# Optimization experiments

Hardware: AMD Instinct MI355X
Metric: run time of the kernel (lower is better)

## Reference

```python
import math
import jax, jax.numpy as jnp
import numpy as np


def get_slopes(n):
    def pow2(n):
        start = 2.0 ** (-(2.0 ** (-(math.log2(n) - 3))))
        return [start * (start ** i) for i in range(n)]
    if math.log2(n).is_integer():
        return pow2(n)
    c = 2 ** math.floor(math.log2(n))
    return pow2(c) + get_slopes(2 * c)[0::2][: n - c]


def setup_inputs() -> dict:
    key = jax.random.key(0)
    B, T, C = 2, 2048, 1024
    ks = jax.random.split(key, 9)
    std = 0.02
    n_layers = 12
    inp = {
        "x": jax.random.normal(ks[0], (B, T, C), dtype=jnp.float32),
        # weights stored as [in, out] (transpose of torch Linear.weight)
        "Wq": std * jax.random.normal(ks[1], (C, C), dtype=jnp.float32),
        "bq": jnp.zeros((C,), dtype=jnp.float32),
        "Wk": std * jax.random.normal(ks[2], (C, C), dtype=jnp.float32),
        "bk": jnp.zeros((C,), dtype=jnp.float32),
        "Wv": std * jax.random.normal(ks[3], (C, C), dtype=jnp.float32),
        "bv": jnp.zeros((C,), dtype=jnp.float32),
        # fc_resid gets std 0.02/sqrt(2*num_layers)
        "Wo": (std / math.sqrt(2 * n_layers)) * jax.random.normal(ks[4], (C, C), dtype=jnp.float32),
        "bo": jnp.zeros((C,), dtype=jnp.float32),
        "n_head": 16,
    }
    return inp


def reference(x, Wq, bq, Wk, bk, Wv, bv, Wo, bo, n_head):
    B, T, C = x.shape
    hd = C // n_head
    # QKV projections, split heads: [B, nh, T, hd]
    def proj(W, b):
        return (x @ W + b).reshape(B, T, n_head, hd).transpose(0, 2, 1, 3)
    q, k, v = proj(Wq, bq), proj(Wk, bk), proj(Wv, bv)

    # ALiBi bias: bias[h, i, j] = -slope_h * (i - j) for j <= i, -inf above diag
    slopes = jnp.asarray(get_slopes(n_head), dtype=x.dtype)  # [nh]
    idx = jnp.arange(T)
    dist = (idx[:, None] - idx[None, :]).astype(x.dtype)  # [T, T], i - j
    bias = -slopes[:, None, None] * dist  # [nh, T, T]
    causal = idx[:, None] >= idx[None, :]
    bias = jnp.where(causal[None], bias, jnp.asarray(-jnp.inf, dtype=x.dtype))

    scale = 1.0 / math.sqrt(hd)
    scores = jnp.einsum("bnqh,bnkh->bnqk", q, k) * scale + bias[None]
    att = jax.nn.softmax(scores, axis=-1)
    y = jnp.einsum("bnqk,bnkh->bnqh", att, v)  # [B, nh, T, hd]
    y = y.transpose(0, 2, 1, 3).reshape(B, T, C)
    return y @ Wo + bo
```

## Files before the change

kernel.cpp:

```cpp
#include <hip/hip_runtime.h>


typedef unsigned short u16;
typedef unsigned int u32;
typedef __attribute__((ext_vector_type(8))) short bf16x8;
typedef __attribute__((ext_vector_type(4))) float f32x4;
typedef __attribute__((ext_vector_type(4))) unsigned short u16x4;

#define MFMA16x16(A, B, C_) __builtin_amdgcn_mfma_f32_16x16x32_bf16((A), (B), (C_), 0, 0, 0)

__device__ __forceinline__ u16 f2bf(float f) {
  u32 x = __builtin_bit_cast(u32, f);
  x += 0x7fff + ((x >> 16) & 1);
  return (u16)(x >> 16);
}

__device__ __forceinline__ void gload_lds16(const u16* g, u16* l) {
  __builtin_amdgcn_global_load_lds(
      (const __attribute__((address_space(1))) void*)g,
      (__attribute__((address_space(3))) void*)l, 16, 0, 0);
}

constexpr int T = 2048, C = 1024, HD = 64;
constexpr int BT = 2 * T;

__device__ __forceinline__ bf16x8 ldsfrag(const u16* lds, int row, int kchunk) {
  return *(const bf16x8*)(lds + row * 64 + (((kchunk) ^ (row & 7)) << 3));
}

__global__ __launch_bounds__(256) void convert_x_kernel(
    const float* __restrict__ xin, u16* __restrict__ xc) {
  int i = (blockIdx.x * 256 + threadIdx.x) * 8;
  const float4 a = *(const float4*)(xin + i);
  const float4 b = *(const float4*)(xin + i + 4);
  uint4 o;
  o.x = (u32)f2bf(a.x) | ((u32)f2bf(a.y) << 16);
  o.y = (u32)f2bf(a.z) | ((u32)f2bf(a.w) << 16);
  o.z = (u32)f2bf(b.x) | ((u32)f2bf(b.y) << 16);
  o.w = (u32)f2bf(b.z) | ((u32)f2bf(b.w) << 16);
  *(uint4*)(xc + i) = o;
}

__global__ __launch_bounds__(256) void transpose4_kernel(
    const float* __restrict__ w0, const float* __restrict__ w1,
    const float* __restrict__ w2, const float* __restrict__ w3,
    u16* __restrict__ wqkvT, u16* __restrict__ woT) {
  __shared__ u16 tile[32][33];
  const int z = blockIdx.z;
  const float* in = (z == 0) ? w0 : (z == 1) ? w1 : (z == 2) ? w2 : w3;
  u16* out = (z < 3) ? (wqkvT + (size_t)z * (1u << 20)) : woT;
  int tx = threadIdx.x, ty = threadIdx.y;
  int x = blockIdx.x * 32 + tx;
#pragma unroll
  for (int i = 0; i < 4; i++) {
    int y = blockIdx.y * 32 + ty + i * 8;
    tile[ty + i * 8][tx] = f2bf(in[y * 1024 + x]);
  }
  __syncthreads();
  int xo = blockIdx.y * 32 + tx;
#pragma unroll
  for (int i = 0; i < 4; i++) {
    int yo = blockIdx.x * 32 + ty + i * 8;
    out[yo * 1024 + xo] = tile[tx][ty + i * 8];
  }
}

__global__ __launch_bounds__(256) void gemm_qkv_kernel(
    const u16* __restrict__ A, const u16* __restrict__ Bt,
    const float* __restrict__ b0, const float* __restrict__ b1,
    const float* __restrict__ b2,
    u16* __restrict__ qout, u16* __restrict__ kout, u16* __restrict__ vtout) {
  constexpr int K = 1024;
  __shared__ __align__(16) u16 As[128 * 64];
  __shared__ __align__(16) u16 Bs[128 * 64];

  const int tid = threadIdx.x;
  const int w = tid >> 6, lane = tid & 63;
  const int l15 = lane & 15, quad = lane >> 4;
  const int m0 = blockIdx.y * 128, n0 = blockIdx.x * 128;
  const int wm = (w >> 1) * 64, wn = (w & 1) * 64;
  const int gsub = (lane & 7) ^ ((lane >> 3) & 7);
  const int rsub = lane >> 3;

  f32x4 acc[4][4] = {};
  const u16* Ag = A + (size_t)m0 * K;
  const u16* Bg = Bt + (size_t)n0 * K;

  for (int k0 = 0; k0 < K; k0 += 64) {
    __syncthreads();
#pragma unroll
    for (int t = 0; t < 4; t++) {
      int rbase = w * 32 + t * 8;
      gload_lds16(Ag + (size_t)(rbase + rsub) * K + k0 + gsub * 8, As + rbase * 64);
      gload_lds16(Bg + (size_t)(rbase + rsub) * K + k0 + gsub * 8, Bs + rbase * 64);
    }
    __syncthreads();
#pragma unroll
    for (int ks = 0; ks < 2; ks++) {
      bf16x8 af[4], bf[4];
#pragma unroll
      for (int mi = 0; mi < 4; mi++)
        af[mi] = ldsfrag(As, wm + mi * 16 + l15, (ks << 2) | quad);
#pragma unroll
      for (int ni = 0; ni < 4; ni++)
        bf[ni] = ldsfrag(Bs, wn + ni * 16 + l15, (ks << 2) | quad);
#pragma unroll
      for (int mi = 0; mi < 4; mi++)
#pragma unroll
        for (int ni = 0; ni < 4; ni++)
          acc[mi][ni] = MFMA16x16(af[mi], bf[ni], acc[mi][ni]);
    }
  }

  const int sel = n0 >> 10;
  const int nloc = n0 & 1023;
  if (sel < 2) {
    u16* D = (sel == 0) ? qout : kout;
    const float* bias = (sel == 0) ? b0 : b1;
#pragma unroll
    for (int mi = 0; mi < 4; mi++)
#pragma unroll
      for (int ni = 0; ni < 4; ni++) {
        int rb = m0 + wm + mi * 16 + quad * 4;
        int col = nloc + wn + ni * 16 + l15;
        float bb = bias[col];
#pragma unroll
        for (int r = 0; r < 4; r++)
          D[(size_t)(rb + r) * 1024 + col] = f2bf(acc[mi][ni][r] + bb);
      }
  } else {
#pragma unroll
    for (int mi = 0; mi < 4; mi++)
#pragma unroll
      for (int ni = 0; ni < 4; ni++) {
        int rb = m0 + wm + mi * 16 + quad * 4;
        int c = nloc + wn + ni * 16 + l15;
        float bb = b2[c];
        u16x4 pk;
#pragma unroll
        for (int r = 0; r < 4; r++) pk[r] = f2bf(acc[mi][ni][r] + bb);
        *(u16x4*)(vtout + (size_t)c * 4096 + rb) = pk;
      }
  }
}

__global__ __launch_bounds__(256) void gemm_out_kernel(
    const u16* __restrict__ A, const u16* __restrict__ Bt,
    const float* __restrict__ bias, float* __restrict__ fout) {
  constexpr int K = 1024;
  __shared__ __align__(16) u16 As[128 * 64];
  __shared__ __align__(16) u16 Bs[64 * 64];

  const int tid = threadIdx.x;
  const int w = tid >> 6, lane = tid & 63;
  const int l15 = lane & 15, quad = lane >> 4;
  const int m0 = blockIdx.y * 128, n0 = blockIdx.x * 64;
  const int wm = (w >> 1) * 64, wn = (w & 1) * 32;
  const int gsub = (lane & 7) ^ ((lane >> 3) & 7);
  const int rsub = lane >> 3;

  f32x4 acc[4][2] = {};
  const u16* Ag = A + (size_t)m0 * K;
  const u16* Bg = Bt + (size_t)n0 * K;

  for (int k0 = 0; k0 < K; k0 += 64) {
    __syncthreads();
#pragma unroll
    for (int t = 0; t < 4; t++) {
      int rbase = w * 32 + t * 8;
      gload_lds16(Ag + (size_t)(rbase + rsub) * K + k0 + gsub * 8, As + rbase * 64);
    }
#pragma unroll
    for (int t = 0; t < 2; t++) {
      int rbase = w * 16 + t * 8;
      gload_lds16(Bg + (size_t)(rbase + rsub) * K + k0 + gsub * 8, Bs + rbase * 64);
    }
    __syncthreads();
#pragma unroll
    for (int ks = 0; ks < 2; ks++) {
      bf16x8 af[4], bf[2];
#pragma unroll
      for (int mi = 0; mi < 4; mi++)
        af[mi] = ldsfrag(As, wm + mi * 16 + l15, (ks << 2) | quad);
#pragma unroll
      for (int ni = 0; ni < 2; ni++)
        bf[ni] = ldsfrag(Bs, wn + ni * 16 + l15, (ks << 2) | quad);
#pragma unroll
      for (int mi = 0; mi < 4; mi++)
#pragma unroll
        for (int ni = 0; ni < 2; ni++)
          acc[mi][ni] = MFMA16x16(af[mi], bf[ni], acc[mi][ni]);
    }
  }

#pragma unroll
  for (int mi = 0; mi < 4; mi++)
#pragma unroll
    for (int ni = 0; ni < 2; ni++) {
      int rb = m0 + wm + mi * 16 + quad * 4;
      int col = n0 + wn + ni * 16 + l15;
      float bb = bias[col];
#pragma unroll
      for (int r = 0; r < 4; r++)
        fout[(size_t)(rb + r) * 1024 + col] = acc[mi][ni][r] + bb;
    }
}

__global__ __launch_bounds__(512, 4) void attn_kernel(
    const u16* __restrict__ qbuf, const u16* __restrict__ kbuf,
    const u16* __restrict__ vtbuf, u16* __restrict__ ybuf) {
  __shared__ __align__(16) u16 Qs[64 * 64];
  __shared__ __align__(16) u16 KVs[4][64 * 64];
  __shared__ __align__(16) u16 Ps[8][16 * 64];

  const int tid = threadIdx.x;
  const int w = tid >> 6, lane = tid & 63;
  const int wq = w & 3, g = w >> 2;
  const int l15 = lane & 15, quad = lane >> 4;
  const int bh = blockIdx.y, b = bh >> 4, h = bh & 15;
  const float slope = exp2f(-0.5f * (float)(h + 1));
  const float slope128 = slope * 128.f;
  const int gsub = (lane & 7) ^ ((lane >> 3) & 7);
  const int rsub = lane >> 3;

  const u16* kbase0 = kbuf + (size_t)b * T * C + h * HD;
  const u16* vtbase0 = vtbuf + (size_t)h * HD * BT + (size_t)b * T;
  u16* Pw = Ps[w];
  const int st = w >> 1;
  const int skind = st & 1;
  const int sjt = st >> 1;
  const int srb = (w & 1) * 32;

#pragma unroll 1
  for (int half = 0; half < 2; half++) {
    const int qt = half == 0 ? (31 - (int)blockIdx.x) : (int)blockIdx.x;

    __syncthreads();
    const u16* qb = qbuf + (size_t)(b * T + qt * 64) * C + h * HD;
    gload_lds16(qb + (size_t)(w * 8 + rsub) * C + gsub * 8, Qs + (w * 8) * 64);
    __syncthreads();
    bf16x8 aq0 = ldsfrag(Qs, wq * 16 + l15, quad);
    bf16x8 aq1 = ldsfrag(Qs, wq * 16 + l15, 4 + quad);

    f32x4 o[4] = {};
    float lsum[4] = {0.f, 0.f, 0.f, 0.f};
    float br[4][4];
    const int ig0 = qt * 64 + wq * 16 + quad * 4;
#pragma unroll
    for (int ni = 0; ni < 4; ni++)
#pragma unroll
      for (int r = 0; r < 4; r++)
        br[ni][r] = slope * (float)(g * 64 + ni * 16 + l15 - ig0 - r);

    const int iters = (qt + 2) >> 1;
#pragma unroll 1
    for (int it = 0; it < iters; it++) {
      __syncthreads();
      {
        int jtv = 2 * it + sjt;
        int jtr = jtv > qt ? qt : jtv;
        const u16* base = skind ? (vtbase0 + jtr * 64)
                                : (kbase0 + (size_t)jtr * 64 * C);
        const int stride = skind ? BT : C;
        u16* dst = KVs[skind * 2 + sjt] + srb * 64;
#pragma unroll
        for (int c2 = 0; c2 < 4; c2++)
          gload_lds16(base + (size_t)(srb + c2 * 8 + rsub) * stride + gsub * 8,
                      dst + c2 * 8 * 64);
      }
      __syncthreads();

      const int jtv = 2 * it + g;
      const u16* Kw = KVs[g];
      const u16* Vw = KVs[2 + g];

      f32x4 s[4];
#pragma unroll
      for (int ni = 0; ni < 4; ni++) {
        bf16x8 kf0 = ldsfrag(Kw, ni * 16 + l15, quad);
        bf16x8 kf1 = ldsfrag(Kw, ni * 16 + l15, 4 + quad);
        f32x4 z = {0.f, 0.f, 0.f, 0.f};
        z = MFMA16x16(aq0, kf0, z);
        z = MFMA16x16(aq1, kf1, z);
        s[ni] = z;
      }

      const bool edge = (jtv >= qt);
#pragma unroll
      for (int ni = 0; ni < 4; ni++)
#pragma unroll
        for (int r = 0; r < 4; r++) {
          float p = __expf(fmaf(s[ni][r], 0.125f, br[ni][r]));
          if (edge && (jtv * 64 + ni * 16 + l15) > (ig0 + r)) p = 0.f;
          lsum[r] += p;
          int prow = quad * 4 + r, pcol = ni * 16 + l15;
          Pw[prow * 64 + (((pcol >> 3) ^ (prow & 7)) << 3) + (pcol & 7)] = f2bf(p);
          br[ni][r] += slope128;
        }

      bf16x8 pa0 = ldsfrag(Pw, l15, quad);
      bf16x8 pa1 = ldsfrag(Pw, l15, 4 + quad);
#pragma unroll
      for (int ni = 0; ni < 4; ni++) {
        bf16x8 vf0 = ldsfrag(Vw, ni * 16 + l15, quad);
        bf16x8 vf1 = ldsfrag(Vw, ni * 16 + l15, 4 + quad);
        o[ni] = MFMA16x16(pa0, vf0, o[ni]);
        o[ni] = MFMA16x16(pa1, vf1, o[ni]);
      }
    }

    __syncthreads();
    float* sc = (float*)KVs;
    float* Osc = sc + wq * 1024;
    float* Lsc = sc + 4096 + wq * 256;
    if (g == 1) {
#pragma unroll
      for (int ni = 0; ni < 4; ni++)
#pragma unroll
        for (int r = 0; r < 4; r++)
          Osc[(quad * 4 + r) * 64 + ni * 16 + l15] = o[ni][r];
#pragma unroll
      for (int r = 0; r < 4; r++)
        Lsc[(quad * 4 + r) * 16 + l15] = lsum[r];
    }
    __syncthreads();
    if (g == 0) {
#pragma unroll
      for (int ni = 0; ni < 4; ni++)
#pragma unroll
        for (int r = 0; r < 4; r++)
          o[ni][r] += Osc[(quad * 4 + r) * 64 + ni * 16 + l15];
#pragma unroll
      for (int r = 0; r < 4; r++) {
        float l = lsum[r] + Lsc[(quad * 4 + r) * 16 + l15];
        l += __shfl_xor(l, 1);
        l += __shfl_xor(l, 2);
        l += __shfl_xor(l, 4);
        l += __shfl_xor(l, 8);
        float inv = 1.f / l;
        int row_g = b * T + qt * 64 + wq * 16 + quad * 4 + r;
        u16* yrow = ybuf + (size_t)row_g * C + h * HD;
#pragma unroll
        for (int ni = 0; ni < 4; ni++)
          yrow[ni * 16 + l15] = f2bf(o[ni][r] * inv);
      }
    }
  }
}

extern "C" void kernel_launch(void* const* d_in, const int* in_sizes, int n_in,
                              void* d_out, int out_size, void* d_ws, size_t ws_size,
                              hipStream_t stream) {
  (void)in_sizes; (void)n_in; (void)out_size; (void)ws_size;
  const float* x  = (const float*)d_in[0];
  const float* Wq = (const float*)d_in[1];
  const float* bq = (const float*)d_in[2];
  const float* Wk = (const float*)d_in[3];
  const float* bk = (const float*)d_in[4];
  const float* Wv = (const float*)d_in[5];
  const float* bv = (const float*)d_in[6];
  const float* Wo = (const float*)d_in[7];
  const float* bo = (const float*)d_in[8];

  u16* ws = (u16*)d_ws;
  constexpr size_t M1 = 1u << 20;
  u16* wqkvT = ws;
  u16* woT   = ws + 3 * M1;
  u16* xc    = ws + 4 * M1;
  u16* qbuf  = ws + 8 * M1;
  u16* vtbuf = ws + 12 * M1;
  u16* kbuf  = (u16*)d_out;
  u16* ybuf  = qbuf;

  convert_x_kernel<<<2048, 256, 0, stream>>>(x, xc);
  transpose4_kernel<<<dim3(32, 32, 4), dim3(32, 8), 0, stream>>>(Wq, Wk, Wv, Wo, wqkvT, woT);
  gemm_qkv_kernel<<<dim3(24, 32), 256, 0, stream>>>(
      xc, wqkvT, bq, bk, bv, qbuf, kbuf, vtbuf);
  attn_kernel<<<dim3(16, 32), 512, 0, stream>>>(qbuf, kbuf, vtbuf, ybuf);
  gemm_out_kernel<<<dim3(16, 32), 256, 0, stream>>>(ybuf, woT, bo, (float*)d_out);
}
```

Measured before the change: 200.0 us.

## Rewrite QKV GEMM with 256x256 tiles and a 4-stage async LDS ring

The QKV projection GEMM moves from 128x128 tiles with 256 threads and a single-buffered LDS load to 256x256 tiles with 512 threads. A four-slot ring of direct global-to-LDS loads keeps three K-steps in flight, gated by explicit vmcnt waits and one barrier per step. It also adds an XOR swizzle on LDS columns, a block-index swizzle for L2 locality, and raised wave priority around the MFMA burst. The aim is to hide global-load latency and raise arithmetic intensity. The cost is far fewer blocks (192) on a large GPU, which risks idle CUs, plus higher register pressure from 32 accumulators per wave.

```diff
diff --git a/kernel.cpp b/kernel.cpp
--- a/kernel.cpp
+++ b/kernel.cpp
@@ -65,51 +65,78 @@
   }
 }
 
-__global__ __launch_bounds__(256) void gemm_qkv_kernel(
+__global__ __launch_bounds__(512, 2) void gemm_qkv_kernel(
     const u16* __restrict__ A, const u16* __restrict__ Bt,
     const float* __restrict__ b0, const float* __restrict__ b1,
     const float* __restrict__ b2,
     u16* __restrict__ qout, u16* __restrict__ kout, u16* __restrict__ vtout) {
-  constexpr int K = 1024;
-  __shared__ __align__(16) u16 As[128 * 64];
-  __shared__ __align__(16) u16 Bs[128 * 64];
+  constexpr int K = 1024, BK = 32, NT = K / BK;
+  __shared__ __align__(16) u16 ring[4][2][256 * BK];
 
   const int tid = threadIdx.x;
   const int w = tid >> 6, lane = tid & 63;
   const int l15 = lane & 15, quad = lane >> 4;
-  const int m0 = blockIdx.y * 128, n0 = blockIdx.x * 128;
-  const int wm = (w >> 1) * 64, wn = (w & 1) * 64;
-  const int gsub = (lane & 7) ^ ((lane >> 3) & 7);
-  const int rsub = lane >> 3;
-
-  f32x4 acc[4][4] = {};
+  const int wr = w >> 2, wc = w & 3;
+  const int bid = blockIdx.y * 12 + blockIdx.x;
+  const int swz = (bid & 7) * 24 + (bid >> 3);
+  const int m0 = (swz / 12) * 256, n0 = (swz % 12) * 256;
+  const int rw = lane >> 2;
+  const int pc = lane & 3;
+
   const u16* Ag = A + (size_t)m0 * K;
   const u16* Bg = Bt + (size_t)n0 * K;
 
-  for (int k0 = 0; k0 < K; k0 += 64) {
-    __syncthreads();
-#pragma unroll
-    for (int t = 0; t < 4; t++) {
-      int rbase = w * 32 + t * 8;
-      gload_lds16(Ag + (size_t)(rbase + rsub) * K + k0 + gsub * 8, As + rbase * 64);
-      gload_lds16(Bg + (size_t)(rbase + rsub) * K + k0 + gsub * 8, Bs + rbase * 64);
-    }
-    __syncthreads();
-#pragma unroll
-    for (int ks = 0; ks < 2; ks++) {
-      bf16x8 af[4], bf[4];
-#pragma unroll
-      for (int mi = 0; mi < 4; mi++)
-        af[mi] = ldsfrag(As, wm + mi * 16 + l15, (ks << 2) | quad);
+  f32x4 acc[8][4] = {};
+
+  auto STAGE = [&](int kt, int s) {
+#pragma unroll
+    for (int j = 0; j < 2; j++) {
+      int row = j * 128 + w * 16 + rw;
+      int cl = pc ^ (row & 3);
+      gload_lds16(Ag + (size_t)row * K + kt * BK + cl * 8,
+                  &ring[s][0][(j * 128 + w * 16) * BK]);
+      gload_lds16(Bg + (size_t)row * K + kt * BK + cl * 8,
+                  &ring[s][1][(j * 128 + w * 16) * BK]);
+    }
+  };
+
+  STAGE(0, 0); STAGE(1, 1); STAGE(2, 2);
+  asm volatile("s_waitcnt vmcnt(8)" ::: "memory");
+  __builtin_amdgcn_s_barrier();
+
+#pragma unroll 1
+  for (int t = 0; t < NT; ++t) {
+    const int s = t & 3;
+    if (t + 3 < NT) STAGE(t + 3, (t + 3) & 3);
+
+    const u16* As = ring[s][0];
+    const u16* Bs = ring[s][1];
+    bf16x8 bfr[4], afr[8];
+#pragma unroll
+    for (int ni = 0; ni < 4; ni++) {
+      int row = wc * 64 + ni * 16 + l15;
+      bfr[ni] = *(const bf16x8*)(Bs + row * BK + ((quad ^ (row & 3)) << 3));
+    }
+#pragma unroll
+    for (int mi = 0; mi < 8; mi++) {
+      int row = wr * 128 + mi * 16 + l15;
+      afr[mi] = *(const bf16x8*)(As + row * BK + ((quad ^ (row & 3)) << 3));
+    }
+    __builtin_amdgcn_s_setprio(1);
+#pragma unroll
+    for (int mi = 0; mi < 8; mi++)
 #pragma unroll
       for (int ni = 0; ni < 4; ni++)
-        bf[ni] = ldsfrag(Bs, wn + ni * 16 + l15, (ks << 2) | quad);
-#pragma unroll
-      for (int mi = 0; mi < 4; mi++)
-#pragma unroll
-        for (int ni = 0; ni < 4; ni++)
-          acc[mi][ni] = MFMA16x16(af[mi], bf[ni], acc[mi][ni]);
-    }
+        acc[mi][ni] = MFMA16x16(afr[mi], bfr[ni], acc[mi][ni]);
+    __builtin_amdgcn_s_setprio(0);
+
+    if (t + 3 < NT)
+      asm volatile("s_waitcnt vmcnt(8)" ::: "memory");
+    else if (t + 2 < NT)
+      asm volatile("s_waitcnt vmcnt(4)" ::: "memory");
+    else if (t + 1 < NT)
+      asm volatile("s_waitcnt vmcnt(0)" ::: "memory");
+    if (t + 1 < NT) __builtin_amdgcn_s_barrier();
   }
 
   const int sel = n0 >> 10;
@@ -118,11 +145,11 @@
     u16* D = (sel == 0) ? qout : kout;
     const float* bias = (sel == 0) ? b0 : b1;
 #pragma unroll
-    for (int mi = 0; mi < 4; mi++)
+    for (int mi = 0; mi < 8; mi++)
 #pragma unroll
       for (int ni = 0; ni < 4; ni++) {
-        int rb = m0 + wm + mi * 16 + quad * 4;
-        int col = nloc + wn + ni * 16 + l15;
+        int rb = m0 + wr * 128 + mi * 16 + quad * 4;
+        int col = nloc + wc * 64 + ni * 16 + l15;
         float bb = bias[col];
 #pragma unroll
         for (int r = 0; r < 4; r++)
@@ -130,11 +157,11 @@
       }
   } else {
 #pragma unroll
-    for (int mi = 0; mi < 4; mi++)
+    for (int mi = 0; mi < 8; mi++)
 #pragma unroll
       for (int ni = 0; ni < 4; ni++) {
-        int rb = m0 + wm + mi * 16 + quad * 4;
-        int c = nloc + wn + ni * 16 + l15;
+        int rb = m0 + wr * 128 + mi * 16 + quad * 4;
+        int c = nloc + wc * 64 + ni * 16 + l15;
         float bb = b2[c];
         u16x4 pk;
 #pragma unroll
@@ -374,7 +401,7 @@
 
   convert_x_kernel<<<2048, 256, 0, stream>>>(x, xc);
   transpose4_kernel<<<dim3(32, 32, 4), dim3(32, 8), 0, stream>>>(Wq, Wk, Wv, Wo, wqkvT, woT);
-  gemm_qkv_kernel<<<dim3(24, 32), 256, 0, stream>>>(
+  gemm_qkv_kernel<<<dim3(12, 16), 512, 0, stream>>>(
       xc, wqkvT, bq, bk, bv, qbuf, kbuf, vtbuf);
   attn_kernel<<<dim3(16, 32), 512, 0, stream>>>(qbuf, kbuf, vtbuf, ybuf);
   gemm_out_kernel<<<dim3(16, 32), 256, 0, stream>>>(ybuf, woT, bo, (float*)d_out);
```

Result: no change. 196.5 us (-1.8%).
